# Optimization experiments

Measured on AMD Instinct MI355X. Metric: run time of the kernel, lower is better.

## Reference

```python
import jax, jax.numpy as jnp
import numpy as np


def setup_inputs() -> dict:
    key = jax.random.key(0)
    k1, k2 = jax.random.split(key)
    x = jax.random.normal(k1, (16, 64, 128, 128), dtype=jnp.float32)
    # 1x1 conv weight, no bias: [C_out, C_in]
    conv_w = jax.random.normal(k2, (64, 64), dtype=jnp.float32) * 0.05
    return {"x": x, "conv_w": conv_w}


def reference(x, conv_w):
    B, C, H, W = x.shape
    N = H * W
    xf = x.reshape(B, C, N)  # [B, C, N]
    # Original: f = X^T X  [B,N,N];  y = X @ (f / N).
    # Mathematically identical reassociation (no nonlinearity between matmuls):
    # y = (X X^T) X / N, using a tiny [B,C,C] gram instead of [B,N,N].
    gram = jnp.einsum('bcn,bdn->bcd', xf, xf) / N  # [B, C, C]
    y = jnp.einsum('bcd,bdn->bcn', gram, xf)       # [B, C, N]
    y = y.reshape(B, C, H, W)
    # 1x1 conv, bias=False: channel mixing
    out = jnp.einsum('oc,bchw->bohw', conv_w, y)
    return out
```

## Files before the change

### kernel.cpp

```cpp
#include <hip/hip_runtime.h>
#include <hip/hip_bf16.h>

#define B_ 16
#define C_ 64
#define N_ 16384
#define KCH 32
#define CPB 512
#define SROW 72

typedef __attribute__((ext_vector_type(8))) short bf16x8;
typedef __attribute__((ext_vector_type(4))) float f32x4;
typedef __attribute__((ext_vector_type(4))) short s16x4;

__device__ __forceinline__ short f2bf(float f) {
    return (short)__bfloat16_as_ushort(__float2bfloat16(f));
}

__device__ __forceinline__ bf16x8 cvt8(float4 lo, float4 hi) {
    bf16x8 r;
    r[0] = f2bf(lo.x); r[1] = f2bf(lo.y); r[2] = f2bf(lo.z); r[3] = f2bf(lo.w);
    r[4] = f2bf(hi.x); r[5] = f2bf(hi.y); r[6] = f2bf(hi.z); r[7] = f2bf(hi.w);
    return r;
}

__global__ __launch_bounds__(256)
void gram_kernel(const float* __restrict__ x, float* __restrict__ gpart) {
    __shared__ float red[2][4096];
    const int t = threadIdx.x, l = t & 63, w = t >> 6;
    const int b = blockIdx.y, ch = blockIdx.x;
    const float* xb = x + (size_t)b * (C_ * (size_t)N_);
    const int row = l & 15, kg = l >> 4;
    const int kbase = ch * CPB + w * (CPB / 4);

    f32x4 acc[4][4] = {};
    float4 raw[2][4][2];

    #pragma unroll
    for (int g = 0; g < 4; ++g) {
        const float* p = xb + (size_t)(16 * g + row) * N_ + kbase + kg * 8;
        raw[0][g][0] = *(const float4*)p;
        raw[0][g][1] = *(const float4*)(p + 4);
    }

    #pragma unroll
    for (int ks = 0; ks < 4; ++ks) {
        const int cb = ks & 1, nb = cb ^ 1;
        if (ks < 3) {
            #pragma unroll
            for (int g = 0; g < 4; ++g) {
                const float* p = xb + (size_t)(16 * g + row) * N_ +
                                 kbase + (ks + 1) * 32 + kg * 8;
                raw[nb][g][0] = *(const float4*)p;
                raw[nb][g][1] = *(const float4*)(p + 4);
            }
        }
        bf16x8 fr[4];
        #pragma unroll
        for (int g = 0; g < 4; ++g) fr[g] = cvt8(raw[cb][g][0], raw[cb][g][1]);
        #pragma unroll
        for (int gc = 0; gc < 4; ++gc)
            #pragma unroll
            for (int gd = 0; gd < 4; ++gd)
                acc[gc][gd] = __builtin_amdgcn_mfma_f32_16x16x32_bf16(
                    fr[gc], fr[gd], acc[gc][gd], 0, 0, 0);
    }

    if (w < 2) {
        #pragma unroll
        for (int gc = 0; gc < 4; ++gc)
            #pragma unroll
            for (int gd = 0; gd < 4; ++gd)
                *(f32x4*)&red[w][(gc * 4 + gd) * 256 + l * 4] = acc[gc][gd];
    }
    __syncthreads();
    if (w >= 2) {
        #pragma unroll
        for (int gc = 0; gc < 4; ++gc)
            #pragma unroll
            for (int gd = 0; gd < 4; ++gd) {
                float* p = &red[w - 2][(gc * 4 + gd) * 256 + l * 4];
                f32x4 v = *(f32x4*)p;
                *(f32x4*)p = v + acc[gc][gd];
            }
    }
    __syncthreads();

    f32x4* dst = (f32x4*)(gpart + ((size_t)b * KCH + ch) * 4096);
    const f32x4* r0 = (const f32x4*)red[0];
    const f32x4* r1 = (const f32x4*)red[1];
    #pragma unroll
    for (int j = 0; j < 4; ++j)
        dst[j * 256 + t] = r0[j * 256 + t] + r1[j * 256 + t];
}

__global__ __launch_bounds__(256)
void rm_kernel(const float* __restrict__ W, const float* __restrict__ gpart,
               unsigned short* __restrict__ Mbf) {
    __shared__ float Gs[C_][17];
    __shared__ float Ws[C_][65];
    const int gd = blockIdx.x, b = blockIdx.y, t = threadIdx.x;

    for (int i = t; i < C_ * C_; i += 256) Ws[i >> 6][i & 63] = W[i];

    const int f = t;
    #pragma unroll
    for (int gc = 0; gc < 4; ++gc) {
        const float* p = gpart + (size_t)b * KCH * 4096 + (gc * 4 + gd) * 256 + f;
        float v[KCH];
        #pragma unroll
        for (int ch = 0; ch < KCH; ++ch)
            v[ch] = p[(size_t)ch * 4096];
        float s = 0.f;
        #pragma unroll
        for (int ch = 0; ch < KCH; ch += 4)
            s += ((v[ch] + v[ch + 1]) + (v[ch + 2] + v[ch + 3]));
        const int c = gc * 16 + (f >> 6) * 4 + (f & 3);
        const int dloc = (f >> 2) & 15;
        Gs[c][dloc] = s;
    }
    __syncthreads();

    const int o = t & 63, g2 = t >> 6;
    const float invN = 1.0f / (float)N_;
    #pragma unroll
    for (int j = 0; j < 4; ++j) {
        const int dloc = g2 * 4 + j;
        float s = 0.f;
        #pragma unroll
        for (int c = 0; c < C_; ++c) s = fmaf(Ws[o][c], Gs[c][dloc], s);
        Mbf[((size_t)b * C_ + o) * C_ + gd * 16 + dloc] = (unsigned short)f2bf(s * invN);
    }
}

__global__ __launch_bounds__(256, 4)
void out_kernel(const float* __restrict__ x, const unsigned short* __restrict__ Mbf,
                float* __restrict__ out) {
    __shared__ unsigned short Xt[256][SROW];
    const int t = threadIdx.x, l = t & 63, w = t >> 6;
    const int b = blockIdx.y, n0 = blockIdx.x * 256;
    const float* xb = x + (size_t)b * (C_ * (size_t)N_);
    const int row = l & 15, kg = l >> 4;

    bf16x8 mfrag[2][4];
    #pragma unroll
    for (int ks = 0; ks < 2; ++ks)
        #pragma unroll
        for (int g = 0; g < 4; ++g)
            mfrag[ks][g] = *(const bf16x8*)((const short*)Mbf +
                ((size_t)b * C_ + 16 * g + row) * C_ + ks * 32 + kg * 8);

    const int d0 = (t & 15) * 4, nb2 = (t >> 4) * 16;
    #pragma unroll
    for (int p = 0; p < 2; ++p) {
        const int n8 = nb2 + p * 8;
        float a[4][8];
        #pragma unroll
        for (int r = 0; r < 4; ++r) {
            const float* src = xb + (size_t)(d0 + r) * N_ + n0 + n8;
            float4 q0 = *(const float4*)src;
            float4 q1 = *(const float4*)(src + 4);
            a[r][0] = q0.x; a[r][1] = q0.y; a[r][2] = q0.z; a[r][3] = q0.w;
            a[r][4] = q1.x; a[r][5] = q1.y; a[r][6] = q1.z; a[r][7] = q1.w;
        }
        #pragma unroll
        for (int j = 0; j < 8; ++j) {
            s16x4 pk;
            pk[0] = f2bf(a[0][j]); pk[1] = f2bf(a[1][j]);
            pk[2] = f2bf(a[2][j]); pk[3] = f2bf(a[3][j]);
            *(s16x4*)&Xt[n8 + j][d0] = pk;
        }
    }
    __syncthreads();

    float* ob = out + (size_t)b * (C_ * (size_t)N_);
    #pragma unroll
    for (int nt = 0; nt < 4; ++nt) {
        const int ntile = w * 4 + nt;
        bf16x8 xfrag0 = *(const bf16x8*)&Xt[ntile * 16 + row][kg * 8];
        bf16x8 xfrag1 = *(const bf16x8*)&Xt[ntile * 16 + row][32 + kg * 8];
        #pragma unroll
        for (int g = 0; g < 4; ++g) {
            f32x4 acc = {};
            acc = __builtin_amdgcn_mfma_f32_16x16x32_bf16(xfrag0, mfrag[0][g], acc, 0, 0, 0);
            acc = __builtin_amdgcn_mfma_f32_16x16x32_bf16(xfrag1, mfrag[1][g], acc, 0, 0, 0);
            __builtin_nontemporal_store(acc,
                (f32x4*)&ob[(size_t)(16 * g + row) * N_ + n0 + ntile * 16 + 4 * kg]);
        }
    }
}

extern "C" void kernel_launch(void* const* d_in, const int* in_sizes, int n_in,
                              void* d_out, int out_size, void* d_ws, size_t ws_size,
                              hipStream_t stream) {
    const float* x = (const float*)d_in[0];
    const float* w = (const float*)d_in[1];
    float* out = (float*)d_out;

    float* gpart = (float*)d_ws;
    unsigned short* Mbf = (unsigned short*)(gpart + (size_t)B_ * KCH * 4096);

    gram_kernel<<<dim3(KCH, B_), 256, 0, stream>>>(x, gpart);
    rm_kernel<<<dim3(4, B_), 256, 0, stream>>>(w, gpart, Mbf);
    out_kernel<<<dim3(N_ / 256, B_), 256, 0, stream>>>(x, Mbf, out);
}
```

Baseline: 51.74 us.

## Fuse gram reduction and mixing into gram kernel via last-block atomic counter

Removes the separate rm_kernel launch. Each gram block now bumps a per-batch atomic counter, and the last block to finish for a batch reduces all partial grams and computes the W·G mixing matrix in shared memory. This saves one kernel launch and its gap, but adds a memset launch. The whole reduction for a batch is serialized onto one block instead of spread over four.

```diff
diff --git a/kernel.cpp b/kernel.cpp
--- a/kernel.cpp
+++ b/kernel.cpp
@@ -23,9 +23,17 @@
     return r;
 }
 
+union __align__(16) GramShared {
+    float red[2][4096];
+    struct { float Gs[C_][65]; float Ws[C_][65]; } rm;
+};
+
 __global__ __launch_bounds__(256)
-void gram_kernel(const float* __restrict__ x, float* __restrict__ gpart) {
-    __shared__ float red[2][4096];
+void gram_kernel(const float* __restrict__ x, const float* __restrict__ W,
+                 float* __restrict__ gpart, unsigned short* __restrict__ Mbf,
+                 int* __restrict__ cnt) {
+    __shared__ GramShared sh;
+    __shared__ int isred;
     const int t = threadIdx.x, l = t & 63, w = t >> 6;
     const int b = blockIdx.y, ch = blockIdx.x;
     const float* xb = x + (size_t)b * (C_ * (size_t)N_);
@@ -70,7 +78,7 @@
         for (int gc = 0; gc < 4; ++gc)
             #pragma unroll
             for (int gd = 0; gd < 4; ++gd)
-                *(f32x4*)&red[w][(gc * 4 + gd) * 256 + l * 4] = acc[gc][gd];
+                *(f32x4*)&sh.red[w][(gc * 4 + gd) * 256 + l * 4] = acc[gc][gd];
     }
     __syncthreads();
     if (w >= 2) {
@@ -78,7 +86,7 @@
         for (int gc = 0; gc < 4; ++gc)
             #pragma unroll
             for (int gd = 0; gd < 4; ++gd) {
-                float* p = &red[w - 2][(gc * 4 + gd) * 256 + l * 4];
+                float* p = &sh.red[w - 2][(gc * 4 + gd) * 256 + l * 4];
                 f32x4 v = *(f32x4*)p;
                 *(f32x4*)p = v + acc[gc][gd];
             }
@@ -86,49 +94,61 @@
     __syncthreads();
 
     f32x4* dst = (f32x4*)(gpart + ((size_t)b * KCH + ch) * 4096);
-    const f32x4* r0 = (const f32x4*)red[0];
-    const f32x4* r1 = (const f32x4*)red[1];
+    const f32x4* r0 = (const f32x4*)sh.red[0];
+    const f32x4* r1 = (const f32x4*)sh.red[1];
     #pragma unroll
     for (int j = 0; j < 4; ++j)
         dst[j * 256 + t] = r0[j * 256 + t] + r1[j * 256 + t];
-}
-
-__global__ __launch_bounds__(256)
-void rm_kernel(const float* __restrict__ W, const float* __restrict__ gpart,
-               unsigned short* __restrict__ Mbf) {
-    __shared__ float Gs[C_][17];
-    __shared__ float Ws[C_][65];
-    const int gd = blockIdx.x, b = blockIdx.y, t = threadIdx.x;
-
-    for (int i = t; i < C_ * C_; i += 256) Ws[i >> 6][i & 63] = W[i];
-
-    const int f = t;
-    #pragma unroll
-    for (int gc = 0; gc < 4; ++gc) {
-        const float* p = gpart + (size_t)b * KCH * 4096 + (gc * 4 + gd) * 256 + f;
-        float v[KCH];
-        #pragma unroll
-        for (int ch = 0; ch < KCH; ++ch)
-            v[ch] = p[(size_t)ch * 4096];
+
+    __threadfence();
+    __syncthreads();
+    if (t == 0) {
+        int old = atomicAdd(&cnt[b], 1);
+        isred = (old == KCH - 1);
+    }
+    __syncthreads();
+    if (!isred) return;
+    __threadfence();
+
+    for (int i = t; i < C_ * C_; i += 256) sh.rm.Ws[i >> 6][i & 63] = W[i];
+
+    const float* gp = gpart + (size_t)b * KCH * 4096;
+    #pragma unroll
+    for (int tp = 0; tp < 8; ++tp) {
+        float v0[KCH], v1[KCH];
+        const float* p0 = gp + (2 * tp + 0) * 256 + t;
+        const float* p1 = gp + (2 * tp + 1) * 256 + t;
+        #pragma unroll
+        for (int ch2 = 0; ch2 < KCH; ++ch2) {
+            v0[ch2] = p0[(size_t)ch2 * 4096];
+            v1[ch2] = p1[(size_t)ch2 * 4096];
+        }
+        float s0 = 0.f, s1 = 0.f;
+        #pragma unroll
+        for (int ch2 = 0; ch2 < KCH; ch2 += 4) {
+            s0 += ((v0[ch2] + v0[ch2 + 1]) + (v0[ch2 + 2] + v0[ch2 + 3]));
+            s1 += ((v1[ch2] + v1[ch2 + 1]) + (v1[ch2 + 2] + v1[ch2 + 3]));
+        }
+        #pragma unroll
+        for (int u = 0; u < 2; ++u) {
+            const int tile = 2 * tp + u;
+            const int gc = tile >> 2, gd = tile & 3;
+            const int c = gc * 16 + (t >> 6) * 4 + (t & 3);
+            const int d = gd * 16 + ((t >> 2) & 15);
+            sh.rm.Gs[c][d] = u ? s1 : s0;
+        }
+    }
+    __syncthreads();
+
+    const int o = t & 63, dg = t >> 6;
+    const float invN = 1.0f / (float)N_;
+    #pragma unroll
+    for (int j = 0; j < 16; ++j) {
+        const int d = dg * 16 + j;
         float s = 0.f;
         #pragma unroll
-        for (int ch = 0; ch < KCH; ch += 4)
-            s += ((v[ch] + v[ch + 1]) + (v[ch + 2] + v[ch + 3]));
-        const int c = gc * 16 + (f >> 6) * 4 + (f & 3);
-        const int dloc = (f >> 2) & 15;
-        Gs[c][dloc] = s;
-    }
-    __syncthreads();
-
-    const int o = t & 63, g2 = t >> 6;
-    const float invN = 1.0f / (float)N_;
-    #pragma unroll
-    for (int j = 0; j < 4; ++j) {
-        const int dloc = g2 * 4 + j;
-        float s = 0.f;
-        #pragma unroll
-        for (int c = 0; c < C_; ++c) s = fmaf(Ws[o][c], Gs[c][dloc], s);
-        Mbf[((size_t)b * C_ + o) * C_ + gd * 16 + dloc] = (unsigned short)f2bf(s * invN);
+        for (int c = 0; c < C_; ++c) s = fmaf(sh.rm.Ws[o][c], sh.rm.Gs[c][d], s);
+        Mbf[((size_t)b * C_ + o) * C_ + d] = (unsigned short)f2bf(s * invN);
     }
 }
 
@@ -198,8 +218,9 @@
 
     float* gpart = (float*)d_ws;
     unsigned short* Mbf = (unsigned short*)(gpart + (size_t)B_ * KCH * 4096);
-
-    gram_kernel<<<dim3(KCH, B_), 256, 0, stream>>>(x, gpart);
-    rm_kernel<<<dim3(4, B_), 256, 0, stream>>>(w, gpart, Mbf);
+    int* cnt = (int*)(Mbf + (size_t)B_ * C_ * C_);
+
+    hipMemsetAsync(cnt, 0, B_ * sizeof(int), stream);
+    gram_kernel<<<dim3(KCH, B_), 256, 0, stream>>>(x, w, gpart, Mbf, cnt);
     out_kernel<<<dim3(N_ / 256, B_), 256, 0, stream>>>(x, Mbf, out);
 }
```

After: 132.3 us. +155.7%, slower.
